# Optimization experiments

Hardware: AMD Instinct MI355X
Metric: run time of the kernel (lower is better)

The kernel has to match this reference:

```python
import jax, jax.numpy as jnp
import numpy as np

W_CHAMFER = 1.0
W_SMOOTH = 0.5
K_NEIGHBORS = 8


def _pairwise_sqdist(a, b):
    # a: [B,N,3], b: [B,M,3] -> [B,N,M] squared euclidean distances
    a2 = jnp.sum(a * a, axis=-1)  # [B,N]
    b2 = jnp.sum(b * b, axis=-1)  # [B,M]
    ab = jnp.einsum('bnd,bmd->bnm', a, b)  # [B,N,M]
    d2 = a2[:, :, None] + b2[:, None, :] - 2.0 * ab
    return jnp.maximum(d2, 0.0)


def _chamfer(pc1, pc2):
    d = jnp.sqrt(_pairwise_sqdist(pc1, pc2))  # [B,N,M] euclidean (matches torch.norm)
    d1 = jnp.min(d, axis=2)  # [B,N]
    d2 = jnp.min(d, axis=1)  # [B,M]
    return jnp.mean(d1) + jnp.mean(d2)


def _smoothness(pc, flow, k=K_NEIGHBORS):
    d2 = _pairwise_sqdist(pc, pc)  # [B,N,N]
    # k+1 nearest (squared dist preserves ordering); drop self (index 0)
    _, idx = jax.lax.top_k(-d2, k + 1)  # [B,N,k+1]
    idx = idx[:, :, 1:]  # [B,N,k]
    neighbor_flow = jax.vmap(lambda f, i: f[i])(flow, idx)  # [B,N,k,3]
    diff = flow[:, :, None, :] - neighbor_flow
    return jnp.mean(jnp.linalg.norm(diff, axis=-1))


def setup_inputs() -> dict:
    key = jax.random.key(0)
    k1, k2, k3 = jax.random.split(key, 3)
    B, N, M = 2, 8192, 8192
    pc1 = jax.random.normal(k1, (B, N, 3), dtype=jnp.float32)
    pc2 = jax.random.normal(k2, (B, M, 3), dtype=jnp.float32)
    pred_flow = jax.random.normal(k3, (B, N, 3), dtype=jnp.float32) * 0.1
    return {"pc1": pc1, "pc2": pc2, "pred_flow": pred_flow}


def reference(pc1, pc2, pred_flow):
    pc1_warped = pc1 + pred_flow
    l_chamfer = _chamfer(pc1_warped, pc2)
    l_smooth = _smoothness(pc1, pred_flow)
    return W_CHAMFER * l_chamfer + W_SMOOTH * l_smooth
```

## Files before the change

### kernel.cpp

```cpp
#include <hip/hip_runtime.h>

#define N_PTS 8192
#define BATCH 2
#define KNN 8
#define NBLK_C 1024
#define NBLK_S 2048
#define NBLOCKS (NBLK_C + NBLK_S)

#define ARR_PC2  0
#define ARR_WARP 2
#define ARR_PC1  4


__device__ __forceinline__ void ce(unsigned &x, unsigned &y) {
    unsigned lo = min(x, y), hi = max(x, y); x = lo; y = hi;
}

__device__ __forceinline__ void insert4(unsigned o[4], unsigned key) {
    unsigned n0 = min(o[0], key);
    unsigned n1 = max(o[0], min(o[1], key));
    unsigned n2 = max(o[1], min(o[2], key));
    unsigned n3 = max(o[2], min(o[3], key));
    o[0]=n0; o[1]=n1; o[2]=n2; o[3]=n3;
}

__device__ __forceinline__ void merge_stage8(unsigned m[8], int d) {
    unsigned p[8], c[8];
    #pragma unroll
    for (int k = 0; k < 8; ++k) p[k] = (unsigned)__shfl_xor((int)m[k], d, 64);
    #pragma unroll
    for (int k = 0; k < 8; ++k) c[k] = min(m[k], p[7-k]);
    ce(c[0],c[4]); ce(c[1],c[5]); ce(c[2],c[6]); ce(c[3],c[7]);
    ce(c[0],c[2]); ce(c[1],c[3]); ce(c[4],c[6]); ce(c[5],c[7]);
    ce(c[0],c[1]); ce(c[2],c[3]); ce(c[4],c[5]); ce(c[6],c[7]);
    #pragma unroll
    for (int k = 0; k < 8; ++k) m[k] = c[k];
}

__device__ __forceinline__ void merge64(unsigned m[8]) {
    merge_stage8(m, 1); merge_stage8(m, 2); merge_stage8(m, 4);
    merge_stage8(m, 8); merge_stage8(m, 16); merge_stage8(m, 32);
}

__global__ __launch_bounds__(256) void pack_kernel(
        const float* __restrict__ pc1, const float* __restrict__ pc2,
        const float* __restrict__ flow, float4* __restrict__ ws) {
    const int t = blockIdx.x * 256 + threadIdx.x;
    const int arr = t >> 13, i = t & (N_PTS - 1);
    const int bb = arr & 1;
    const size_t base = (size_t)bb * N_PTS * 3 + (size_t)i * 3;
    float x, y, z;
    if (arr < 2)      { x = pc2[base+0];              y = pc2[base+1];              z = pc2[base+2]; }
    else if (arr < 4) { x = pc1[base+0] + flow[base+0];
                        y = pc1[base+1] + flow[base+1];
                        z = pc1[base+2] + flow[base+2]; }
    else              { x = pc1[base+0];              y = pc1[base+1];              z = pc1[base+2]; }
    ws[t] = make_float4(x, y, z, fmaf(x, x, fmaf(y, y, z * z)));
}

__global__ __launch_bounds__(256, 4) void mega_kernel(
        const float4* __restrict__ ws, const float* __restrict__ flow,
        float* __restrict__ out) {
    __shared__ float psum[4];
    const int tid = threadIdx.x, bx = blockIdx.x;
    const int lane = tid & 63, wv = tid >> 6;
    const int ri = bx / 3, role = bx % 3;

    if (role == 2) {
        const int z = ri >> 8, bb = z & 1, dir = z >> 1;
        const int cb = ri & 255;
        const float4* rows = ws + (size_t)((dir == 0 ? ARR_WARP : ARR_PC2) + bb) * N_PTS;
        const float4* cand = ws + (size_t)((dir == 0 ? ARR_PC2 : ARR_WARP) + bb) * N_PTS;
        const int rbase = cb * 32 + wv * 8;

        float mx[8], my[8], mz[8], bmin[8];
        #pragma unroll
        for (int k = 0; k < 8; ++k) {
            float4 q = rows[rbase + k];
            mx[k] = -2.0f * q.x; my[k] = -2.0f * q.y; mz[k] = -2.0f * q.z;
            bmin[k] = __builtin_inff();
        }

        #pragma unroll 2
        for (int j = 0; j < N_PTS; j += 128) {
            float4 qa = cand[j + lane];
            float4 qb = cand[j + 64 + lane];
            #pragma unroll
            for (int k = 0; k < 8; ++k) {
                float sa = fmaf(mx[k], qa.x, fmaf(my[k], qa.y, fmaf(mz[k], qa.z, qa.w)));
                float sb = fmaf(mx[k], qb.x, fmaf(my[k], qb.y, fmaf(mz[k], qb.z, qb.w)));
                bmin[k] = fminf(fminf(bmin[k], sa), sb);
            }
        }

        #pragma unroll
        for (int k = 0; k < 8; ++k) {
            #pragma unroll
            for (int d = 1; d < 64; d <<= 1)
                bmin[k] = fminf(bmin[k], __shfl_xor(bmin[k], d, 64));
        }
        if (lane == 0) {
            float val = 0.0f;
            #pragma unroll
            for (int k = 0; k < 8; ++k) {
                float p2k = 0.25f * fmaf(mx[k], mx[k], fmaf(my[k], my[k], mz[k] * mz[k]));
                val += sqrtf(fmaxf(bmin[k] + p2k, 0.0f));
            }
            psum[wv] = val;
        }
        __syncthreads();
        if (tid == 0) {
            float ch = psum[0] + psum[1] + psum[2] + psum[3];
            atomicAdd(out, ch * (1.0f / (float)(BATCH * N_PTS)));
        }
    } else {
        const int sbx = ri * 2 + role;
        const int b  = sbx >> 10;
        const int sx = sbx & 1023;
        const int i0w = sx * 8 + wv * 2;
        const float4* cand = ws + (size_t)(ARR_PC1 + b) * N_PTS;
        const float* F = flow + (size_t)b * N_PTS * 3;

        float mx[2], my[2], mz[2], p2[2], gr[2];
        unsigned thr[2], o[2][4];
        #pragma unroll
        for (int r = 0; r < 2; ++r) {
            float4 q = cand[i0w + r];
            mx[r] = -2.0f * q.x; my[r] = -2.0f * q.y; mz[r] = -2.0f * q.z;
            p2[r] = q.w;
            gr[r] = __builtin_inff();
            thr[r] = 0xFFFFFFFFu;
            #pragma unroll
            for (int k = 0; k < 4; ++k) o[r][k] = 0xFFFFFFFFu;
        }

        auto update_thr = [&]() {
            #pragma unroll
            for (int r = 0; r < 2; ++r) {
                unsigned m0 = o[r][0], m1 = o[r][1], m2 = o[r][2], m3 = o[r][3];
                #pragma unroll
                for (int d = 1; d <= 16; d <<= 1) {
                    unsigned q0 = (unsigned)__shfl_xor((int)m0, d, 64);
                    unsigned q1 = (unsigned)__shfl_xor((int)m1, d, 64);
                    unsigned q2 = (unsigned)__shfl_xor((int)m2, d, 64);
                    unsigned q3 = (unsigned)__shfl_xor((int)m3, d, 64);
                    unsigned c0 = min(m0, q3), c1 = min(m1, q2);
                    unsigned c2 = min(m2, q1), c3 = min(m3, q0);
                    ce(c0, c2); ce(c1, c3); ce(c0, c1); ce(c2, c3);
                    m0 = c0; m1 = c1; m2 = c2; m3 = c3;
                }
                unsigned bound = max(m3, (unsigned)__shfl_xor((int)m3, 32, 64));
                thr[r] = min(thr[r], bound);
                float thr_up = __uint_as_float((thr[r] & 0xFFFFE000u) + 0x4000u);
                gr[r] = thr_up - p2[r];
            }
        };

        auto gated_span = [&](int j0, int j1) {
            #pragma unroll 2
            for (int j = j0; j < j1; j += 128) {
                float4 qa = cand[j + lane];
                float4 qb = cand[j + 64 + lane];
                int ja = j + lane, jb = j + 64 + lane;
                float sa[2], sb[2];
                #pragma unroll
                for (int r = 0; r < 2; ++r) {
                    sa[r] = fmaf(mx[r], qa.x, fmaf(my[r], qa.y, fmaf(mz[r], qa.z, qa.w)));
                    sb[r] = fmaf(mx[r], qb.x, fmaf(my[r], qb.y, fmaf(mz[r], qb.z, qb.w)));
                }
                #pragma unroll
                for (int r = 0; r < 2; ++r) {
                    if (__any(fminf(sa[r], sb[r]) <= gr[r])) {
                        float da = fmaxf(sa[r] + p2[r], 0.0f);
                        unsigned ka = (__float_as_uint(da) & 0xFFFFE000u) | (unsigned)ja;
                        ka = (ja == i0w + r) ? 0xFFFFFFFFu : ka;
                        insert4(o[r], ka);
                        float db = fmaxf(sb[r] + p2[r], 0.0f);
                        unsigned kb = (__float_as_uint(db) & 0xFFFFE000u) | (unsigned)jb;
                        kb = (jb == i0w + r) ? 0xFFFFFFFFu : kb;
                        insert4(o[r], kb);
                    }
                }
            }
        };

        #pragma unroll 2
        for (int j = 0; j < 1024; j += 128) {
            float4 qa = cand[j + lane];
            float4 qb = cand[j + 64 + lane];
            int ja = j + lane, jb = j + 64 + lane;
            #pragma unroll
            for (int r = 0; r < 2; ++r) {
                float sa = fmaf(mx[r], qa.x, fmaf(my[r], qa.y, fmaf(mz[r], qa.z, qa.w)));
                float da = fmaxf(sa + p2[r], 0.0f);
                unsigned ka = (__float_as_uint(da) & 0xFFFFE000u) | (unsigned)ja;
                ka = (ja == i0w + r) ? 0xFFFFFFFFu : ka;
                insert4(o[r], ka);
                float sb = fmaf(mx[r], qb.x, fmaf(my[r], qb.y, fmaf(mz[r], qb.z, qb.w)));
                float db = fmaxf(sb + p2[r], 0.0f);
                unsigned kb = (__float_as_uint(db) & 0xFFFFE000u) | (unsigned)jb;
                kb = (jb == i0w + r) ? 0xFFFFFFFFu : kb;
                insert4(o[r], kb);
            }
        }
        update_thr();
        gated_span(1024, 2048); update_thr();
        gated_span(2048, 4096); update_thr();
        gated_span(4096, N_PTS);

        const int sel = lane & 15;
        const int pr = sel >> 3, kk = sel & 7;
        unsigned mykey = 0xFFFFFFFFu;
        #pragma unroll
        for (int r = 0; r < 2; ++r) {
            unsigned m[8] = {o[r][0], o[r][1], o[r][2], o[r][3],
                             0xFFFFFFFFu, 0xFFFFFFFFu, 0xFFFFFFFFu, 0xFFFFFFFFu};
            merge64(m);
            if (pr == r) {
                unsigned k2 = m[0];
                #pragma unroll
                for (int t = 1; t < 8; ++t) k2 = (kk == t) ? m[t] : k2;
                mykey = k2;
            }
        }
        const int i = i0w + pr;
        const int j = (int)(mykey & (N_PTS - 1));
        float dx = F[i*3+0] - F[j*3+0];
        float dy = F[i*3+1] - F[j*3+1];
        float dz = F[i*3+2] - F[j*3+2];
        float sv = sqrtf(fmaf(dx, dx, fmaf(dy, dy, dz * dz)));
        #pragma unroll
        for (int d = 1; d < 64; d <<= 1) sv += __shfl_xor(sv, d, 64);
        if (lane == 0) psum[wv] = sv;
        __syncthreads();

        if (tid == 0) {
            float sm = psum[0] + psum[1] + psum[2] + psum[3];
            atomicAdd(out, sm * (0.125f / ((float)BATCH * N_PTS * KNN)));
        }
    }
}

extern "C" void kernel_launch(void* const* d_in, const int* in_sizes, int n_in,
                              void* d_out, int out_size, void* d_ws, size_t ws_size,
                              hipStream_t stream) {
    const float* pc1  = (const float*)d_in[0];
    const float* pc2  = (const float*)d_in[1];
    const float* flow = (const float*)d_in[2];
    float* out = (float*)d_out;
    float4* ws4 = (float4*)d_ws;

    pack_kernel<<<dim3(6 * N_PTS / 256), 256, 0, stream>>>(pc1, pc2, flow, ws4);
    mega_kernel<<<dim3(NBLOCKS), 256, 0, stream>>>(ws4, flow, out);
}
```

Measured before the change: 136.2 us.

## Restructure chamfer to row-per-lane with split candidates; 4 rows per kNN wave

The chamfer blocks now give each lane one query row. Each wave scans a quarter of the candidates with wave-uniform (broadcast) loads, and the four partial minima are combined through shared memory. This replaces the per-wave 8-row scheme that needed a 64-lane shuffle reduction for every row. The kNN smoothness waves now process 4 query rows instead of 2, which doubles reuse of each loaded candidate and halves the block counts. The cost is more registers per thread, which may lower occupancy, and fewer blocks for load balancing.

```diff
diff --git a/kernel.cpp b/kernel.cpp
--- a/kernel.cpp
+++ b/kernel.cpp
@@ -3,8 +3,8 @@
 #define N_PTS 8192
 #define BATCH 2
 #define KNN 8
-#define NBLK_C 1024
-#define NBLK_S 2048
+#define NBLK_C 512
+#define NBLK_S 1024
 #define NBLOCKS (NBLK_C + NBLK_S)
 
 #define ARR_PC2  0
@@ -61,70 +61,55 @@
 __global__ __launch_bounds__(256, 4) void mega_kernel(
         const float4* __restrict__ ws, const float* __restrict__ flow,
         float* __restrict__ out) {
+    __shared__ float cmin[4][64];
     __shared__ float psum[4];
     const int tid = threadIdx.x, bx = blockIdx.x;
     const int lane = tid & 63, wv = tid >> 6;
     const int ri = bx / 3, role = bx % 3;
 
     if (role == 2) {
-        const int z = ri >> 8, bb = z & 1, dir = z >> 1;
-        const int cb = ri & 255;
+        const int z = ri >> 7, bb = z & 1, dir = z >> 1;
+        const int cb = ri & 127;
         const float4* rows = ws + (size_t)((dir == 0 ? ARR_WARP : ARR_PC2) + bb) * N_PTS;
         const float4* cand = ws + (size_t)((dir == 0 ? ARR_PC2 : ARR_WARP) + bb) * N_PTS;
-        const int rbase = cb * 32 + wv * 8;
-
-        float mx[8], my[8], mz[8], bmin[8];
-        #pragma unroll
-        for (int k = 0; k < 8; ++k) {
-            float4 q = rows[rbase + k];
-            mx[k] = -2.0f * q.x; my[k] = -2.0f * q.y; mz[k] = -2.0f * q.z;
-            bmin[k] = __builtin_inff();
-        }
-
-        #pragma unroll 2
-        for (int j = 0; j < N_PTS; j += 128) {
-            float4 qa = cand[j + lane];
-            float4 qb = cand[j + 64 + lane];
-            #pragma unroll
-            for (int k = 0; k < 8; ++k) {
-                float sa = fmaf(mx[k], qa.x, fmaf(my[k], qa.y, fmaf(mz[k], qa.z, qa.w)));
-                float sb = fmaf(mx[k], qb.x, fmaf(my[k], qb.y, fmaf(mz[k], qb.z, qb.w)));
-                bmin[k] = fminf(fminf(bmin[k], sa), sb);
-            }
-        }
-
-        #pragma unroll
-        for (int k = 0; k < 8; ++k) {
-            #pragma unroll
-            for (int d = 1; d < 64; d <<= 1)
-                bmin[k] = fminf(bmin[k], __shfl_xor(bmin[k], d, 64));
-        }
-        if (lane == 0) {
-            float val = 0.0f;
-            #pragma unroll
-            for (int k = 0; k < 8; ++k) {
-                float p2k = 0.25f * fmaf(mx[k], mx[k], fmaf(my[k], my[k], mz[k] * mz[k]));
-                val += sqrtf(fmaxf(bmin[k] + p2k, 0.0f));
-            }
-            psum[wv] = val;
-        }
+
+        float4 q = rows[cb * 64 + lane];
+        const float mx = -2.0f * q.x, my = -2.0f * q.y, mz = -2.0f * q.z;
+        const float p2 = q.w;
+        float bmin = __builtin_inff();
+
+        const int wvu = __builtin_amdgcn_readfirstlane(wv);
+        const int j0 = wvu * 2048;
+        #pragma unroll 8
+        for (int j = j0; j < j0 + 2048; j += 2) {
+            float4 ca = cand[j];
+            float4 cb4 = cand[j + 1];
+            float sa = fmaf(mx, ca.x,  fmaf(my, ca.y,  fmaf(mz, ca.z,  ca.w)));
+            float sb = fmaf(mx, cb4.x, fmaf(my, cb4.y, fmaf(mz, cb4.z, cb4.w)));
+            bmin = fminf(fminf(bmin, sa), sb);
+        }
+        cmin[wv][lane] = bmin;
         __syncthreads();
-        if (tid == 0) {
-            float ch = psum[0] + psum[1] + psum[2] + psum[3];
-            atomicAdd(out, ch * (1.0f / (float)(BATCH * N_PTS)));
+        if (wv == 0) {
+            float m = fminf(fminf(cmin[0][lane], cmin[1][lane]),
+                            fminf(cmin[2][lane], cmin[3][lane]));
+            float val = sqrtf(fmaxf(m + p2, 0.0f));
+            #pragma unroll
+            for (int d = 1; d < 64; d <<= 1) val += __shfl_xor(val, d, 64);
+            if (lane == 0) atomicAdd(out, val * (1.0f / (float)(BATCH * N_PTS)));
         }
     } else {
         const int sbx = ri * 2 + role;
-        const int b  = sbx >> 10;
-        const int sx = sbx & 1023;
-        const int i0w = sx * 8 + wv * 2;
+        const int b  = sbx >> 9;
+        const int sx = sbx & 511;
+        const int i0w = sx * 16 + wv * 4;
         const float4* cand = ws + (size_t)(ARR_PC1 + b) * N_PTS;
         const float* F = flow + (size_t)b * N_PTS * 3;
 
-        float mx[2], my[2], mz[2], p2[2], gr[2];
-        unsigned thr[2], o[2][4];
+        float mx[4], my[4], mz[4], p2[4], gr[4];
+        unsigned thr[4], o[4][4];
         #pragma unroll
-        for (int r = 0; r < 2; ++r) {
+        for (int r = 0; r < 4; ++r) {
             float4 q = cand[i0w + r];
             mx[r] = -2.0f * q.x; my[r] = -2.0f * q.y; mz[r] = -2.0f * q.z;
             p2[r] = q.w;
@@ -136,7 +121,7 @@
 
         auto update_thr = [&]() {
             #pragma unroll
-            for (int r = 0; r < 2; ++r) {
+            for (int r = 0; r < 4; ++r) {
                 unsigned m0 = o[r][0], m1 = o[r][1], m2 = o[r][2], m3 = o[r][3];
                 #pragma unroll
                 for (int d = 1; d <= 16; d <<= 1) {
@@ -162,14 +147,14 @@
                 float4 qa = cand[j + lane];
                 float4 qb = cand[j + 64 + lane];
                 int ja = j + lane, jb = j + 64 + lane;
-                float sa[2], sb[2];
-                #pragma unroll
-                for (int r = 0; r < 2; ++r) {
+                float sa[4], sb[4];
+                #pragma unroll
+                for (int r = 0; r < 4; ++r) {
                     sa[r] = fmaf(mx[r], qa.x, fmaf(my[r], qa.y, fmaf(mz[r], qa.z, qa.w)));
                     sb[r] = fmaf(mx[r], qb.x, fmaf(my[r], qb.y, fmaf(mz[r], qb.z, qb.w)));
                 }
                 #pragma unroll
-                for (int r = 0; r < 2; ++r) {
+                for (int r = 0; r < 4; ++r) {
                     if (__any(fminf(sa[r], sb[r]) <= gr[r])) {
                         float da = fmaxf(sa[r] + p2[r], 0.0f);
                         unsigned ka = (__float_as_uint(da) & 0xFFFFE000u) | (unsigned)ja;
@@ -190,7 +175,7 @@
             float4 qb = cand[j + 64 + lane];
             int ja = j + lane, jb = j + 64 + lane;
             #pragma unroll
-            for (int r = 0; r < 2; ++r) {
+            for (int r = 0; r < 4; ++r) {
                 float sa = fmaf(mx[r], qa.x, fmaf(my[r], qa.y, fmaf(mz[r], qa.z, qa.w)));
                 float da = fmaxf(sa + p2[r], 0.0f);
                 unsigned ka = (__float_as_uint(da) & 0xFFFFE000u) | (unsigned)ja;
@@ -208,11 +193,11 @@
         gated_span(2048, 4096); update_thr();
         gated_span(4096, N_PTS);
 
-        const int sel = lane & 15;
+        const int sel = lane & 31;
         const int pr = sel >> 3, kk = sel & 7;
         unsigned mykey = 0xFFFFFFFFu;
         #pragma unroll
-        for (int r = 0; r < 2; ++r) {
+        for (int r = 0; r < 4; ++r) {
             unsigned m[8] = {o[r][0], o[r][1], o[r][2], o[r][3],
                              0xFFFFFFFFu, 0xFFFFFFFFu, 0xFFFFFFFFu, 0xFFFFFFFFu};
             merge64(m);
@@ -236,7 +221,7 @@
 
         if (tid == 0) {
             float sm = psum[0] + psum[1] + psum[2] + psum[3];
-            atomicAdd(out, sm * (0.125f / ((float)BATCH * N_PTS * KNN)));
+            atomicAdd(out, sm * (0.25f / ((float)BATCH * N_PTS * KNN)));
         }
     }
 }
```

Result: slower. 144.4 us (+6.0%).
